# Optimization experiments

Hardware: AMD Instinct MI355X
Metric: run time of the kernel (lower is better)

The kernel has to match this reference:

```python
import jax, jax.numpy as jnp
import numpy as np

HID = 1024
HEADS = 16
HEAD_DIM = HID // HEADS


def setup_inputs() -> dict:
    key = jax.random.key(0)
    ks = jax.random.split(key, 11)
    s = 1.0 / np.sqrt(HID)
    return {
        "query": jax.random.normal(ks[0], (4, 2048, HID), jnp.float32),
        "key": jax.random.normal(ks[1], (4, 2048, HID), jnp.float32),
        "value": jax.random.normal(ks[2], (4, 2048, HID), jnp.float32),
        "wq": jax.random.normal(ks[3], (HID, HID), jnp.float32) * s,
        "bq": jnp.zeros((HID,), jnp.float32),
        "wk": jax.random.normal(ks[4], (HID, HID), jnp.float32) * s,
        "bk": jnp.zeros((HID,), jnp.float32),
        "wv": jax.random.normal(ks[5], (HID, HID), jnp.float32) * s,
        "bv": jnp.zeros((HID,), jnp.float32),
        "wo": jax.random.normal(ks[6], (HID, HID), jnp.float32) * s,
        "bo": jnp.zeros((HID,), jnp.float32),
    }


def reference(query, key, value, wq, bq, wk, bk, wv, bv, wo, bo):
    b, s, _ = query.shape
    scale = jnp.sqrt(jnp.asarray(HEAD_DIM, query.dtype))
    # linear projections; weights stored as [in, out]
    Q = (query @ wq + bq).reshape(b, s, HEADS, HEAD_DIM).transpose(0, 2, 1, 3)
    K = (key @ wk + bk).reshape(b, s, HEADS, HEAD_DIM).transpose(0, 2, 1, 3)
    V = (value @ wv + bv).reshape(b, s, HEADS, HEAD_DIM).transpose(0, 2, 1, 3)
    energy = jnp.einsum('bhqd,bhkd->bhqk', Q, K) / scale  # [B,H,S,S]
    attention = jax.nn.softmax(energy, axis=-1)  # dropout p=0 -> identity
    x = jnp.einsum('bhqk,bhkd->bhqd', attention, V)
    x = x.transpose(0, 2, 1, 3).reshape(b, s, HID)
    return x @ wo + bo
```

## Files before the change

### kernel.cpp

```cpp
#include <hip/hip_runtime.h>
#include <hip/hip_bf16.h>

#define B_   4
#define S_   2048
#define HID_ 1024
#define H_   16
#define D_   64
#define M_   (B_ * S_)

typedef __attribute__((ext_vector_type(8)))  short bf16x8;
typedef __attribute__((ext_vector_type(4)))  float f32x4;
typedef __attribute__((ext_vector_type(16))) float f32x16;

#define GAS __attribute__((address_space(1)))
#define LAS __attribute__((address_space(3)))

__device__ __forceinline__ unsigned short f2bf(float f) {
    union { float f; unsigned int u; } x; x.f = f;
    unsigned int u = x.u;
    return (unsigned short)((u + 0x7fffu + ((u >> 16) & 1u)) >> 16);
}

__global__ __launch_bounds__(256)
void cast3(const float* __restrict__ q, const float* __restrict__ k, const float* __restrict__ v,
           unsigned short* __restrict__ oq, unsigned short* __restrict__ ok,
           unsigned short* __restrict__ ov) {
    const int sel = blockIdx.x >> 12;
    const int i = (blockIdx.x & 4095) * 256 + threadIdx.x;
    const float* in = (sel == 0) ? q : (sel == 1) ? k : v;
    unsigned short* out = (sel == 0) ? oq : (sel == 1) ? ok : ov;
    const f32x4 a = ((const f32x4*)in)[i * 2];
    const f32x4 b = ((const f32x4*)in)[i * 2 + 1];
    bf16x8 w;
#pragma unroll
    for (int j = 0; j < 4; j++) { w[j] = (short)f2bf(a[j]); w[4 + j] = (short)f2bf(b[j]); }
    ((bf16x8*)out)[i] = w;
}

__global__ void transpose_cast(const float* __restrict__ w0, const float* __restrict__ w1,
                               const float* __restrict__ w2, const float* __restrict__ w3,
                               unsigned short* __restrict__ o0, unsigned short* __restrict__ o1,
                               unsigned short* __restrict__ o2, unsigned short* __restrict__ o3) {
    __shared__ float t[32][33];
    const float* w = (blockIdx.z == 0) ? w0 : (blockIdx.z == 1) ? w1 : (blockIdx.z == 2) ? w2 : w3;
    unsigned short* o = (blockIdx.z == 0) ? o0 : (blockIdx.z == 1) ? o1 : (blockIdx.z == 2) ? o2 : o3;
    const int tx = threadIdx.x, ty = threadIdx.y;
    const int bx = blockIdx.x * 32, by = blockIdx.y * 32;
#pragma unroll
    for (int i = 0; i < 4; i++)
        t[ty + i * 8][tx] = w[(size_t)(by + ty + i * 8) * HID_ + bx + tx];
    __syncthreads();
#pragma unroll
    for (int i = 0; i < 4; i++)
        o[(size_t)(bx + ty + i * 8) * HID_ + by + tx] = f2bf(t[tx][ty + i * 8]);
}

__global__ __launch_bounds__(256, 4)
void gemm_qkv(const unsigned short* __restrict__ aq, const unsigned short* __restrict__ ak,
              const unsigned short* __restrict__ av, const unsigned short* __restrict__ wqkvT,
              const float* __restrict__ bq, const float* __restrict__ bk,
              const float* __restrict__ bv, unsigned short* __restrict__ Qp,
              unsigned short* __restrict__ Kp, unsigned short* __restrict__ Vt, float cvt) {
    constexpr int BK = 32;
    constexpr int NT = HID_ / BK;
    __shared__ unsigned short smem[2][8192];

    const int tid  = threadIdx.x;
    const int lane = tid & 63;
    const int wave = tid >> 6;
    const int quad = lane >> 4;
    const int col  = lane & 15;
    const int wr   = (wave & 1) * 64;
    const int wc   = (wave >> 1) * 64;
    const int m0   = blockIdx.x * 128;
    const int third = blockIdx.y >> 3;
    const int n0l   = (blockIdx.y & 7) * 128;
    const bool vmode = (third == 2);

    const unsigned short* act = (third == 0) ? aq : (third == 1) ? ak : av;
    const float* bias = (third == 0) ? bq : (third == 1) ? bk : bv;
    unsigned short* outp = (third == 0) ? Qp : (third == 1) ? Kp : Vt;
    const float oscale = (third == 0) ? cvt : 1.f;

    const int grow = wave * 16 + (lane >> 2);
    const int gcol = (lane & 3) * 8;
    const unsigned short* wgp = wqkvT + (size_t)(third * HID_ + n0l + grow) * HID_ + gcol;
    const unsigned short* agp = act + (size_t)(m0 + grow) * HID_ + gcol;
    const unsigned short* rgp = vmode ? agp : wgp;
    const unsigned short* cgp = vmode ? wgp : agp;

    auto stage = [&](int buf, int kt) {
        unsigned short* as_ = &smem[buf][wave * 512];
        unsigned short* bs_ = &smem[buf][4096 + wave * 512];
        __builtin_amdgcn_global_load_lds((const GAS unsigned int*)(rgp + kt),
                                         (LAS unsigned int*)as_, 16, 0, 0);
        __builtin_amdgcn_global_load_lds((const GAS unsigned int*)(rgp + kt + (size_t)64 * HID_),
                                         (LAS unsigned int*)(as_ + 2048), 16, 0, 0);
        __builtin_amdgcn_global_load_lds((const GAS unsigned int*)(cgp + kt),
                                         (LAS unsigned int*)bs_, 16, 0, 0);
        __builtin_amdgcn_global_load_lds((const GAS unsigned int*)(cgp + kt + (size_t)64 * HID_),
                                         (LAS unsigned int*)(bs_ + 2048), 16, 0, 0);
    };

    f32x4 zero; zero[0] = 0.f; zero[1] = 0.f; zero[2] = 0.f; zero[3] = 0.f;
    f32x4 acc[4][4];
#pragma unroll
    for (int ri = 0; ri < 4; ri++)
#pragma unroll
        for (int ci = 0; ci < 4; ci++) acc[ri][ci] = zero;

    stage(0, 0);
    __syncthreads();

    for (int t = 0; t < NT; ++t) {
        const int cur = t & 1;
        if (t + 1 < NT) stage(cur ^ 1, (t + 1) * BK);
        const unsigned short* Asc = smem[cur];
        const unsigned short* Bsc = smem[cur] + 4096;
        bf16x8 af[4], cf[4];
#pragma unroll
        for (int i = 0; i < 4; i++) af[i] = *(const bf16x8*)&Asc[(wr + i * 16 + col) * BK + quad * 8];
#pragma unroll
        for (int i = 0; i < 4; i++) cf[i] = *(const bf16x8*)&Bsc[(wc + i * 16 + col) * BK + quad * 8];
#pragma unroll
        for (int ri = 0; ri < 4; ri++)
#pragma unroll
            for (int ci = 0; ci < 4; ci++)
                acc[ri][ci] = __builtin_amdgcn_mfma_f32_16x16x32_bf16(af[ri], cf[ci], acc[ri][ci], 0, 0, 0);
        __syncthreads();
    }

    unsigned short* RB = &smem[0][0];
#pragma unroll
    for (int ph = 0; ph < 2; ph++) {
        if ((wave >> 1) == ph) {
#pragma unroll
            for (int ri = 0; ri < 4; ri++) {
                f32x4 bv4;
                if (!vmode) bv4 = *(const f32x4*)&bias[n0l + wr + ri * 16 + quad * 4];
#pragma unroll
                for (int ci = 0; ci < 4; ci++) {
                    float b0, b1, b2, b3;
                    if (!vmode) { b0 = bv4[0]; b1 = bv4[1]; b2 = bv4[2]; b3 = bv4[3]; }
                    else { b0 = b1 = b2 = b3 = bias[n0l + wc + ci * 16 + col]; }
                    const unsigned int u0 = f2bf((acc[ri][ci][0] + b0) * oscale);
                    const unsigned int u1 = f2bf((acc[ri][ci][1] + b1) * oscale);
                    const unsigned int u2 = f2bf((acc[ri][ci][2] + b2) * oscale);
                    const unsigned int u3 = f2bf((acc[ri][ci][3] + b3) * oscale);
                    uint2 w; w.x = u0 | (u1 << 16); w.y = u2 | (u3 << 16);
                    *(uint2*)&RB[(ci * 16 + col) * 136 + wr + ri * 16 + quad * 4] = w;
                }
            }
        }
        __syncthreads();
#pragma unroll
        for (int it = 0; it < 4; it++) {
            const int c   = it * 256 + tid;
            const int row = c >> 4, ch = c & 15;
            const bf16x8 v = *(const bf16x8*)&RB[row * 136 + ch * 8];
            if (!vmode) {
                const int n = n0l + ch * 8;
                const int h = n >> 6, d = n & 63;
                const int m = m0 + ph * 64 + row;
                *(bf16x8*)&outp[(((size_t)(m >> 11) * H_ + h) * S_ + (m & 2047)) * D_ + d] = v;
            } else {
                const int m = m0 + ch * 8;
                const int n = n0l + ph * 64 + row;
                const int h = n >> 6, d = n & 63;
                *(bf16x8*)&outp[(((size_t)(m >> 11) * H_ + h) * D_ + d) * S_ + (m & 2047)] = v;
            }
        }
        __syncthreads();
    }
}

__global__ __launch_bounds__(256, 4)
void gemm_o(const unsigned short* __restrict__ A, const unsigned short* __restrict__ Bt,
            const float* __restrict__ bias, float* __restrict__ outp) {
    constexpr int BK = 32;
    constexpr int NT = HID_ / BK;
    __shared__ float smemf[64 * 132];
    unsigned short* sb = (unsigned short*)smemf;

    const int tid  = threadIdx.x;
    const int lane = tid & 63;
    const int wave = tid >> 6;
    const int quad = lane >> 4;
    const int col  = lane & 15;
    const int wn   = (wave >> 1) * 64;
    const int wm   = (wave & 1) * 64;
    const int m0   = blockIdx.x * 128;
    const int n0l  = blockIdx.y * 128;

    const int grow = wave * 16 + (lane >> 2);
    const int gcol = (lane & 3) * 8;
    const unsigned short* agp = A + (size_t)(m0 + grow) * HID_ + gcol;
    const unsigned short* wgp = Bt + (size_t)(n0l + grow) * HID_ + gcol;

    auto stage = [&](int buf, int kt) {
        unsigned short* as_ = sb + buf * 8192 + wave * 512;
        unsigned short* bs_ = sb + buf * 8192 + 4096 + wave * 512;
        __builtin_amdgcn_global_load_lds((const GAS unsigned int*)(wgp + kt),
                                         (LAS unsigned int*)as_, 16, 0, 0);
        __builtin_amdgcn_global_load_lds((const GAS unsigned int*)(wgp + kt + (size_t)64 * HID_),
                                         (LAS unsigned int*)(as_ + 2048), 16, 0, 0);
        __builtin_amdgcn_global_load_lds((const GAS unsigned int*)(agp + kt),
                                         (LAS unsigned int*)bs_, 16, 0, 0);
        __builtin_amdgcn_global_load_lds((const GAS unsigned int*)(agp + kt + (size_t)64 * HID_),
                                         (LAS unsigned int*)(bs_ + 2048), 16, 0, 0);
    };

    f32x4 zero; zero[0] = 0.f; zero[1] = 0.f; zero[2] = 0.f; zero[3] = 0.f;
    f32x4 acc[4][4];
#pragma unroll
    for (int ri = 0; ri < 4; ri++)
#pragma unroll
        for (int ci = 0; ci < 4; ci++) acc[ri][ci] = zero;

    stage(0, 0);
    __syncthreads();

    for (int t = 0; t < NT; ++t) {
        const int cur = t & 1;
        if (t + 1 < NT) stage(cur ^ 1, (t + 1) * BK);
        const unsigned short* Asc = sb + cur * 8192;
        const unsigned short* Bsc = Asc + 4096;
        bf16x8 wf[4], af[4];
#pragma unroll
        for (int i = 0; i < 4; i++) wf[i] = *(const bf16x8*)&Asc[(wn + i * 16 + col) * BK + quad * 8];
#pragma unroll
        for (int i = 0; i < 4; i++) af[i] = *(const bf16x8*)&Bsc[(wm + i * 16 + col) * BK + quad * 8];
#pragma unroll
        for (int ri = 0; ri < 4; ri++)
#pragma unroll
            for (int ci = 0; ci < 4; ci++)
                acc[ri][ci] = __builtin_amdgcn_mfma_f32_16x16x32_bf16(wf[ri], af[ci], acc[ri][ci], 0, 0, 0);
        __syncthreads();
    }

#pragma unroll
    for (int ph = 0; ph < 2; ph++) {
        if ((wave & 1) == ph) {
#pragma unroll
            for (int ri = 0; ri < 4; ri++) {
                const f32x4 bv4 = *(const f32x4*)&bias[n0l + wn + ri * 16 + quad * 4];
#pragma unroll
                for (int ci = 0; ci < 4; ci++) {
                    f32x4 v;
#pragma unroll
                    for (int i = 0; i < 4; i++) v[i] = acc[ri][ci][i] + bv4[i];
                    *(f32x4*)&smemf[(ci * 16 + col) * 132 + wn + ri * 16 + quad * 4] = v;
                }
            }
        }
        __syncthreads();
#pragma unroll
        for (int it = 0; it < 8; it++) {
            const int c   = it * 256 + tid;
            const int row = c >> 5, ch = c & 31;
            const f32x4 v = *(const f32x4*)&smemf[row * 132 + ch * 4];
            *(f32x4*)&outp[(size_t)(m0 + ph * 64 + row) * HID_ + n0l + ch * 4] = v;
        }
        __syncthreads();
    }
}

__global__ __launch_bounds__(256, 4)
void attn_k(const unsigned short* __restrict__ Qp, const unsigned short* __restrict__ Kp,
            const unsigned short* __restrict__ Vt, unsigned short* __restrict__ Xc) {
    constexpr int LT = 72;
    constexpr int NT = S_ / 64;
    __shared__ unsigned short Ks[2][64 * LT];
    __shared__ unsigned short Vs[2][64 * LT];

    const int tid  = threadIdx.x;
    const int lane = tid & 63;
    const int wave = tid >> 6;
    const int l31  = lane & 31;
    const int hw   = lane >> 5;
    const int bh   = blockIdx.y;
    const int q0   = blockIdx.x * 128 + wave * 32;

    const unsigned short* Qb = Qp + (size_t)bh * S_ * D_;
    const unsigned short* Kb = Kp + (size_t)bh * S_ * D_;
    const unsigned short* Vb = Vt + (size_t)bh * D_ * S_;

    bf16x8 qf[4];
#pragma unroll
    for (int ks = 0; ks < 4; ks++)
        qf[ks] = *(const bf16x8*)&Qb[(q0 + l31) * D_ + ks * 16 + hw * 8];

    f32x16 o[2];
#pragma unroll
    for (int t = 0; t < 2; t++)
#pragma unroll
        for (int i = 0; i < 16; i++) o[t][i] = 0.f;
    float lpart = 0.f;

    const int srow = tid >> 3;
    const int seg  = (tid & 7) * 8;
    bf16x8 kr[2], vr[2];

#pragma unroll
    for (int it = 0; it < 2; it++) {
        const int row = it * 32 + srow;
        kr[it] = *(const bf16x8*)&Kb[(size_t)row * D_ + seg];
        vr[it] = *(const bf16x8*)&Vb[(size_t)row * S_ + seg];
    }
#pragma unroll
    for (int it = 0; it < 2; it++) {
        const int row = it * 32 + srow;
        *(bf16x8*)&Ks[0][row * LT + seg] = kr[it];
        *(bf16x8*)&Vs[0][row * LT + seg] = vr[it];
    }
#pragma unroll
    for (int it = 0; it < 2; it++) {
        const int row = it * 32 + srow;
        kr[it] = *(const bf16x8*)&Kb[(size_t)(64 + row) * D_ + seg];
        vr[it] = *(const bf16x8*)&Vb[(size_t)row * S_ + 64 + seg];
    }
    __syncthreads();

    for (int t = 0; t < NT; ++t) {
        const int cur = t & 1;
#pragma unroll
        for (int g = 0; g < 2; g++) {
            f32x16 e;
#pragma unroll
            for (int i = 0; i < 16; i++) e[i] = 0.f;
#pragma unroll
            for (int ks = 0; ks < 4; ks++) {
                const bf16x8 a = *(const bf16x8*)&Ks[cur][(g * 32 + l31) * LT + ks * 16 + hw * 8];
                e = __builtin_amdgcn_mfma_f32_32x32x16_bf16(a, qf[ks], e, 0, 0, 0);
            }
            unsigned int ulo[4], uhi[4];
#pragma unroll
            for (int grp = 0; grp < 4; grp++) {
                const float p0 = __builtin_amdgcn_exp2f(e[grp * 4 + 0]);
                const float p1 = __builtin_amdgcn_exp2f(e[grp * 4 + 1]);
                const float p2 = __builtin_amdgcn_exp2f(e[grp * 4 + 2]);
                const float p3 = __builtin_amdgcn_exp2f(e[grp * 4 + 3]);
                lpart += (p0 + p1) + (p2 + p3);
                asm("v_cvt_pk_bf16_f32 %0, %1, %2" : "=v"(ulo[grp]) : "v"(p0), "v"(p1));
                asm("v_cvt_pk_bf16_f32 %0, %1, %2" : "=v"(uhi[grp]) : "v"(p2), "v"(p3));
            }
#pragma unroll
            for (int sub = 0; sub < 2; sub++) {
                unsigned int w0 = ulo[2 * sub], w2 = ulo[2 * sub + 1];
                unsigned int w1 = uhi[2 * sub], w3 = uhi[2 * sub + 1];
                asm("v_permlane32_swap_b32 %0, %1" : "+v"(w0), "+v"(w2));
                asm("v_permlane32_swap_b32 %0, %1" : "+v"(w1), "+v"(w3));
                union { unsigned int u[4]; bf16x8 v; } pf;
                pf.u[0] = w0; pf.u[1] = w1; pf.u[2] = w2; pf.u[3] = w3;
                const int ks = g * 2 + sub;
#pragma unroll
                for (int tt = 0; tt < 2; tt++) {
                    const bf16x8 vf = *(const bf16x8*)&Vs[cur][(tt * 32 + l31) * LT + ks * 16 + hw * 8];
                    o[tt] = __builtin_amdgcn_mfma_f32_32x32x16_bf16(vf, pf.v, o[tt], 0, 0, 0);
                }
            }
        }

        if (t + 1 < NT) {
#pragma unroll
            for (int it = 0; it < 2; it++) {
                const int row = it * 32 + srow;
                *(bf16x8*)&Ks[cur ^ 1][row * LT + seg] = kr[it];
                *(bf16x8*)&Vs[cur ^ 1][row * LT + seg] = vr[it];
            }
            if (t + 2 < NT) {
                const int c0 = (t + 2) * 64;
#pragma unroll
                for (int it = 0; it < 2; it++) {
                    const int row = it * 32 + srow;
                    kr[it] = *(const bf16x8*)&Kb[(size_t)(c0 + row) * D_ + seg];
                    vr[it] = *(const bf16x8*)&Vb[(size_t)row * S_ + c0 + seg];
                }
            }
        }
        __syncthreads();
    }

    float l = lpart;
    l += __shfl_xor(l, 32);
    const float inv = 1.f / l;

    const int b = bh >> 4, h = bh & 15;
    const int s = q0 + l31;
    unsigned short* xp = &Xc[((size_t)(b * S_ + s)) * HID_ + h * D_];
#pragma unroll
    for (int t = 0; t < 2; t++)
#pragma unroll
        for (int grp = 0; grp < 4; grp++) {
            const unsigned int u0 = f2bf(o[t][grp * 4 + 0] * inv);
            const unsigned int u1 = f2bf(o[t][grp * 4 + 1] * inv);
            const unsigned int u2 = f2bf(o[t][grp * 4 + 2] * inv);
            const unsigned int u3 = f2bf(o[t][grp * 4 + 3] * inv);
            uint2 w; w.x = u0 | (u1 << 16); w.y = u2 | (u3 << 16);
            *(uint2*)&xp[t * 32 + grp * 8 + hw * 4] = w;
        }
}

extern "C" void kernel_launch(void* const* d_in, const int* in_sizes, int n_in,
                              void* d_out, int out_size, void* d_ws, size_t ws_size,
                              hipStream_t stream) {
    (void)in_sizes; (void)n_in; (void)out_size; (void)ws_size;
    const float* query = (const float*)d_in[0];
    const float* key   = (const float*)d_in[1];
    const float* value = (const float*)d_in[2];
    const float* wq    = (const float*)d_in[3];
    const float* bq    = (const float*)d_in[4];
    const float* wk    = (const float*)d_in[5];
    const float* bk    = (const float*)d_in[6];
    const float* wv    = (const float*)d_in[7];
    const float* bv    = (const float*)d_in[8];
    const float* wo    = (const float*)d_in[9];
    const float* bo    = (const float*)d_in[10];
    float* out = (float*)d_out;

    unsigned short* ws  = (unsigned short*)d_ws;
    const size_t WSZ = (size_t)HID_ * HID_;
    const size_t TSZ = (size_t)M_ * HID_;
    unsigned short* wqkvT = ws;
    unsigned short* woT = ws + 3 * WSZ;
    unsigned short* Qp  = woT + WSZ;
    unsigned short* Kp  = Qp + TSZ;
    unsigned short* Vt  = Kp + TSZ;
    unsigned short* Xc  = Vt + TSZ;
    unsigned short* Xb  = Xc + TSZ;

    const float cvt = 0.125f * 1.44269504f;

    transpose_cast<<<dim3(32, 32, 4), dim3(32, 8), 0, stream>>>(
        wq, wk, wv, wo, wqkvT, wqkvT + WSZ, wqkvT + 2 * WSZ, woT);

    cast3<<<3 * 4096, 256, 0, stream>>>(query, key, value, Xc, Xb, Xb + TSZ);

    gemm_qkv<<<dim3(M_ / 128, 24), 256, 0, stream>>>(
        Xc, Xb, Xb + TSZ, wqkvT, bq, bk, bv, Qp, Kp, Vt, cvt);

    attn_k<<<dim3(S_ / 128, B_ * H_), 256, 0, stream>>>(Qp, Kp, Vt, Xc);

    gemm_o<<<dim3(M_ / 128, 8), 256, 0, stream>>>(Xc, woT, bo, out);
}
```

Baseline: 337.9 us.

## Merge prep kernels and remap block IDs for XCD-aware L2 locality

Merges the activation cast and the weight transpose-cast into a single prep launch, saving one kernel launch. Remaps linear block IDs in gemm_qkv, gemm_o and attn_k so that blocks landing on the same XCD (round-robin by lb&7) share the same weight column tiles or the same attention heads. The aim is better L2 reuse within each XCD's private L2. The swizzle stays correct only while the grid dimensions divide evenly into the assumed 8x8 and 8x16 groupings.

```diff
diff --git a/kernel.cpp b/kernel.cpp
--- a/kernel.cpp
+++ b/kernel.cpp
@@ -22,37 +22,41 @@
 }
 
 __global__ __launch_bounds__(256)
-void cast3(const float* __restrict__ q, const float* __restrict__ k, const float* __restrict__ v,
-           unsigned short* __restrict__ oq, unsigned short* __restrict__ ok,
-           unsigned short* __restrict__ ov) {
-    const int sel = blockIdx.x >> 12;
-    const int i = (blockIdx.x & 4095) * 256 + threadIdx.x;
-    const float* in = (sel == 0) ? q : (sel == 1) ? k : v;
-    unsigned short* out = (sel == 0) ? oq : (sel == 1) ? ok : ov;
-    const f32x4 a = ((const f32x4*)in)[i * 2];
-    const f32x4 b = ((const f32x4*)in)[i * 2 + 1];
-    bf16x8 w;
-#pragma unroll
-    for (int j = 0; j < 4; j++) { w[j] = (short)f2bf(a[j]); w[4 + j] = (short)f2bf(b[j]); }
-    ((bf16x8*)out)[i] = w;
-}
-
-__global__ void transpose_cast(const float* __restrict__ w0, const float* __restrict__ w1,
-                               const float* __restrict__ w2, const float* __restrict__ w3,
-                               unsigned short* __restrict__ o0, unsigned short* __restrict__ o1,
-                               unsigned short* __restrict__ o2, unsigned short* __restrict__ o3) {
+void prep(const float* __restrict__ q, const float* __restrict__ k, const float* __restrict__ v,
+          unsigned short* __restrict__ oq, unsigned short* __restrict__ ok,
+          unsigned short* __restrict__ ov,
+          const float* __restrict__ w0, const float* __restrict__ w1,
+          const float* __restrict__ w2, const float* __restrict__ w3,
+          unsigned short* __restrict__ t0, unsigned short* __restrict__ t1,
+          unsigned short* __restrict__ t2, unsigned short* __restrict__ t3) {
     __shared__ float t[32][33];
-    const float* w = (blockIdx.z == 0) ? w0 : (blockIdx.z == 1) ? w1 : (blockIdx.z == 2) ? w2 : w3;
-    unsigned short* o = (blockIdx.z == 0) ? o0 : (blockIdx.z == 1) ? o1 : (blockIdx.z == 2) ? o2 : o3;
-    const int tx = threadIdx.x, ty = threadIdx.y;
-    const int bx = blockIdx.x * 32, by = blockIdx.y * 32;
-#pragma unroll
-    for (int i = 0; i < 4; i++)
-        t[ty + i * 8][tx] = w[(size_t)(by + ty + i * 8) * HID_ + bx + tx];
-    __syncthreads();
-#pragma unroll
-    for (int i = 0; i < 4; i++)
-        o[(size_t)(bx + ty + i * 8) * HID_ + by + tx] = f2bf(t[tx][ty + i * 8]);
+    const int tid = threadIdx.x;
+    if (blockIdx.x < 12288) {
+        const int sel = blockIdx.x >> 12;
+        const int i = (blockIdx.x & 4095) * 256 + tid;
+        const float* in = (sel == 0) ? q : (sel == 1) ? k : v;
+        unsigned short* out = (sel == 0) ? oq : (sel == 1) ? ok : ov;
+        const f32x4 a = ((const f32x4*)in)[i * 2];
+        const f32x4 b = ((const f32x4*)in)[i * 2 + 1];
+        bf16x8 w;
+#pragma unroll
+        for (int j = 0; j < 4; j++) { w[j] = (short)f2bf(a[j]); w[4 + j] = (short)f2bf(b[j]); }
+        ((bf16x8*)out)[i] = w;
+    } else {
+        const int tb = blockIdx.x - 12288;
+        const int z = tb >> 10, rem = tb & 1023;
+        const int bx = (rem & 31) * 32, by = (rem >> 5) * 32;
+        const int tx = tid & 31, ty = tid >> 5;
+        const float* w = (z == 0) ? w0 : (z == 1) ? w1 : (z == 2) ? w2 : w3;
+        unsigned short* o = (z == 0) ? t0 : (z == 1) ? t1 : (z == 2) ? t2 : t3;
+#pragma unroll
+        for (int i = 0; i < 4; i++)
+            t[ty + i * 8][tx] = w[(size_t)(by + ty + i * 8) * HID_ + bx + tx];
+        __syncthreads();
+#pragma unroll
+        for (int i = 0; i < 4; i++)
+            o[(size_t)(bx + ty + i * 8) * HID_ + by + tx] = f2bf(t[tx][ty + i * 8]);
+    }
 }
 
 __global__ __launch_bounds__(256, 4)
@@ -72,9 +76,14 @@
     const int col  = lane & 15;
     const int wr   = (wave & 1) * 64;
     const int wc   = (wave >> 1) * 64;
-    const int m0   = blockIdx.x * 128;
-    const int third = blockIdx.y >> 3;
-    const int n0l   = (blockIdx.y & 7) * 128;
+
+    const int lb = blockIdx.x + gridDim.x * blockIdx.y;
+    const int r8 = lb & 7, qq = lb >> 3;
+    const int bx = r8 * 8 + (qq & 7);
+    const int by = qq >> 3;
+    const int m0   = bx * 128;
+    const int third = by >> 3;
+    const int n0l   = (by & 7) * 128;
     const bool vmode = (third == 2);
 
     const unsigned short* act = (third == 0) ? aq : (third == 1) ? ak : av;
@@ -189,8 +198,11 @@
     const int col  = lane & 15;
     const int wn   = (wave >> 1) * 64;
     const int wm   = (wave & 1) * 64;
-    const int m0   = blockIdx.x * 128;
-    const int n0l  = blockIdx.y * 128;
+
+    const int lb = blockIdx.x + gridDim.x * blockIdx.y;
+    const int r8 = lb & 7, qq = lb >> 3;
+    const int m0  = (r8 * 8 + (qq & 7)) * 128;
+    const int n0l = (qq >> 3) * 128;
 
     const int grow = wave * 16 + (lane >> 2);
     const int gcol = (lane & 3) * 8;
@@ -278,8 +290,11 @@
     const int wave = tid >> 6;
     const int l31  = lane & 31;
     const int hw   = lane >> 5;
-    const int bh   = blockIdx.y;
-    const int q0   = blockIdx.x * 128 + wave * 32;
+
+    const int lb = blockIdx.x + gridDim.x * blockIdx.y;
+    const int r8 = lb & 7, qq = lb >> 3;
+    const int bh = r8 + 8 * (qq >> 4);
+    const int q0 = (qq & 15) * 128 + wave * 32;
 
     const unsigned short* Qb = Qp + (size_t)bh * S_ * D_;
     const unsigned short* Kb = Kp + (size_t)bh * S_ * D_;
@@ -431,10 +446,9 @@
 
     const float cvt = 0.125f * 1.44269504f;
 
-    transpose_cast<<<dim3(32, 32, 4), dim3(32, 8), 0, stream>>>(
+    prep<<<16384, 256, 0, stream>>>(
+        query, key, value, Xc, Xb, Xb + TSZ,
         wq, wk, wv, wo, wqkvT, wqkvT + WSZ, wqkvT + 2 * WSZ, woT);
-
-    cast3<<<3 * 4096, 256, 0, stream>>>(query, key, value, Xc, Xb, Xb + TSZ);
 
     gemm_qkv<<<dim3(M_ / 128, 24), 256, 0, stream>>>(
         Xc, Xb, Xb + TSZ, wqkvT, bq, bk, bv, Qp, Kp, Vt, cvt);
```

New measurement: 333.1 us. About the same (-1.4%).
